# Performance work log

Measured on AMD Instinct MI355X. Metric: run time of the kernel, lower is better.

## Reference

```python
import jax, jax.numpy as jnp
import numpy as np
from jax import lax

V, D_IN, H, B, T = 80, 8, 256, 4096, 80
W_SCALE = 1.0 / np.sqrt(H)  # matches torch nn.LSTM uniform init scale


def setup_inputs() -> dict:
    key = jax.random.key(0)
    ks = jax.random.split(key, 8)
    inp = {
        "x": jax.random.randint(ks[0], (B, T), 0, V),
        "h0": jnp.zeros((2, B, H), jnp.float32),
        "c0": jnp.zeros((2, B, H), jnp.float32),
        "emb": jax.random.normal(ks[1], (V, D_IN), jnp.float32),
        "W_ih0": jax.random.normal(ks[2], (4 * H, D_IN), jnp.float32) * W_SCALE,
        "W_hh0": jax.random.normal(ks[3], (4 * H, H), jnp.float32) * W_SCALE,
        "W_ih1": jax.random.normal(ks[4], (4 * H, H), jnp.float32) * W_SCALE,
        "W_hh1": jax.random.normal(ks[5], (4 * H, H), jnp.float32) * W_SCALE,
        "fc_W": jax.random.normal(ks[6], (V, H), jnp.float32) * W_SCALE,
        "fc_b": jnp.zeros((V,), jnp.float32),
    }
    return inp


def _lstm_layer(xs, h0, c0, W_ih, W_hh):
    # xs: [T, B, d_in]; precompute input contribution for all timesteps at once
    x_gates = jnp.einsum("tbd,gd->tbg", xs, W_ih)  # [T, B, 4H]

    def step(carry, xg):
        h, c = carry
        gates = xg + h @ W_hh.T  # [B, 4H], torch gate order i,f,g,o
        i, f, g, o = jnp.split(gates, 4, axis=-1)
        c = jax.nn.sigmoid(f) * c + jax.nn.sigmoid(i) * jnp.tanh(g)
        h = jax.nn.sigmoid(o) * jnp.tanh(c)
        return (h, c), h

    (hT, cT), hs = lax.scan(step, (h0, c0), x_gates)
    return hs, hT, cT  # hs: [T, B, H]


def reference(x, h0, c0, emb, W_ih0, W_hh0, W_ih1, W_hh1, fc_W, fc_b):
    xe = emb[x]                     # [B, T, D_IN] embedding lookup
    xs = jnp.swapaxes(xe, 0, 1)     # [T, B, D_IN] time-major for scan
    h1s, h1T, c1T = _lstm_layer(xs, h0[0], c0[0], W_ih0, W_hh0)
    h2s, h2T, c2T = _lstm_layer(h1s, h0[1], c0[1], W_ih1, W_hh1)
    logits = h2s[-1] @ fc_W.T + fc_b            # fc on last timestep: [B, V]
    h_n = jnp.stack([h1T, h2T])                  # [2, B, H]
    c_n = jnp.stack([c1T, c2T])
    return logits, h_n, c_n
```

## Files before the change

kernel.cpp:

```cpp
#include <hip/hip_runtime.h>
#include <hip/hip_bf16.h>
#include <stdint.h>

typedef __bf16 bf16x8 __attribute__((ext_vector_type(8)));
typedef float  f32x4  __attribute__((ext_vector_type(4)));

#define MFMA16(a, b, c) __builtin_amdgcn_mfma_f32_16x16x32_bf16((a), (b), (c), 0, 0, 0)

namespace {
constexpr int T_   = 80;
constexpr int B_   = 4096;
constexpr int H_   = 256;
constexpr int HP_  = 264;
constexpr int V_   = 80;
constexpr int RF   = 16;
constexpr int RC   = 32;
constexpr int NH   = 128;
constexpr int NTILE = 128;
constexpr int OUT_HN = B_ * V_;
constexpr int OUT_CN = OUT_HN + 2 * B_ * H_;

constexpr size_t WB_WHH0 = 0;
constexpr size_t WB_WIH1 = (size_t)1 << 20;
constexpr size_t WB_WHH1 = (size_t)2 << 20;
constexpr size_t WB_WIH0 = (size_t)3 << 20;
constexpr int WS_PLANE = 794624;
constexpr size_t WSB_XCHG  = 3178496;
constexpr size_t XCHG_U32  = (size_t)RC * NH;
constexpr size_t WSB_FLAGS = WSB_XCHG + (size_t)2 * 2 * NTILE * 2 * XCHG_U32 * 4;
constexpr int    CTRL_U32  = 512 + 256 + 8;
constexpr size_t WSB_TOTAL = WSB_FLAGS + (size_t)CTRL_U32 * 4;
}

__device__ __forceinline__ float sigm_(float x) { return 1.0f / (1.0f + __expf(-x)); }
__device__ __forceinline__ float tanh_(float x) {
  x = fminf(fmaxf(x, -15.f), 15.f);
  float e = __expf(2.f * x);
  return (e - 1.f) / (e + 1.f);
}

__device__ __forceinline__ void split_(float w, __hip_bfloat16* hi, __hip_bfloat16* lo) {
  __hip_bfloat16 h = __float2bfloat16(w);
  *hi = h;
  *lo = __float2bfloat16(w - __bfloat162float(h));
}

__device__ __forceinline__ uint32_t pack2_(__hip_bfloat16 hi, __hip_bfloat16 lo) {
  return (uint32_t)__builtin_bit_cast(unsigned short, hi) |
         ((uint32_t)__builtin_bit_cast(unsigned short, lo) << 16);
}
__device__ __forceinline__ __hip_bfloat16 ubf_(unsigned short v) {
  return __builtin_bit_cast(__hip_bfloat16, v);
}

__device__ __forceinline__ void ldfrag_(const char* pp, bf16x8* h, bf16x8* l) {
  *h = *(const bf16x8*)pp;
  *l = *(const bf16x8*)(pp + 16);
}

__device__ __forceinline__ size_t addrK256_(int e) {
  int row = e >> 8, kk = e & 255;
  int g = row >> 8, cb = row & 255, t = cb >> 4, m = cb & 15;
  int k = kk >> 5, quad = (kk >> 3) & 3, j = kk & 7;
  return (size_t)(((t * 8 + k) * 4 + g)) * 2048 + (size_t)((quad * 16 + m) * 32 + j * 2);
}

__global__ __launch_bounds__(256) void cvt_pair(
    const float* __restrict__ Wih0f, const float* __restrict__ Whh0f,
    const float* __restrict__ Wih1f, const float* __restrict__ Whh1f,
    __hip_bfloat16* __restrict__ ws, int zero_flags)
{
  if (zero_flags && blockIdx.x < 4) {
    uint32_t* fl = (uint32_t*)((char*)ws + WSB_FLAGS);
    int idx = blockIdx.x * 256 + threadIdx.x;
    if (idx < CTRL_U32) fl[idx] = 0u;
  }
  int i = blockIdx.x * 256 + threadIdx.x;
  if (i >= WS_PLANE) return;
  char* wb = (char*)ws;
  float v; size_t off;
  if (i < 262144) {
    v = Whh0f[i];            off = WB_WHH0 + addrK256_(i);
  } else if (i < 524288) {
    int e = i - 262144;
    v = Wih1f[e];            off = WB_WIH1 + addrK256_(e);
  } else if (i < 786432) {
    int e = i - 524288;
    v = Whh1f[e];            off = WB_WHH1 + addrK256_(e);
  } else {
    int e = i - 786432;
    int row = e >> 3, j = e & 7;
    int g = row >> 8, cb = row & 255, t = cb >> 4, m = cb & 15;
    v = Wih0f[e];
    off = WB_WIH0 + (size_t)((t * 4 + g) * 512 + m * 32 + j * 2);
  }
  __hip_bfloat16 hi = __float2bfloat16(v);
  *(__hip_bfloat16*)(wb + off)      = hi;
  *(__hip_bfloat16*)(wb + off + 16) = __float2bfloat16(v - __bfloat162float(hi));
}

__device__ __forceinline__ f32x4 tri_(bf16x8 ahi, bf16x8 alo, bf16x8 bhi, bf16x8 blo, f32x4 acc) {
  acc = MFMA16(ahi, bhi, acc);
  acc = MFMA16(ahi, blo, acc);
  acc = MFMA16(alo, bhi, acc);
  return acc;
}

__global__ __attribute__((amdgpu_waves_per_eu(2, 2))) __launch_bounds__(512)
void lstm_coop(
    const int* __restrict__ x,
    const float* __restrict__ h0,
    const float* __restrict__ c0,
    const float* __restrict__ emb,
    const __hip_bfloat16* __restrict__ wsW,
    const float* __restrict__ fcW,
    const float* __restrict__ fcb,
    float* __restrict__ out)
{
  __shared__ __align__(16) __hip_bfloat16 h1s[2][2][RC][HP_];
  __shared__ __align__(16) __hip_bfloat16 h2s[2][RC][HP_];
  __shared__ __align__(16) __hip_bfloat16 embs[2][V_][8];
  __shared__ unsigned short toks[RC][T_];
  __shared__ int slot_s;

  const int tid  = threadIdx.x;
  const int lane = tid & 63;
  const int wv   = tid >> 6;
  const int m    = lane & 15;
  const int quad = lane >> 4;
  const int jw   = wv * 16;
  const int lane32 = lane << 5;

  uint32_t* xch   = (uint32_t*)((char*)wsW + WSB_XCHG);
  uint32_t* flags = (uint32_t*)((char*)wsW + WSB_FLAGS);
  uint32_t* owner = flags + 512;
  uint32_t* cnt   = flags + 768;

  if (tid == 0) {
    uint32_t xcd;
    asm volatile("s_getreg_b32 %0, hwreg(20, 0, 4)" : "=s"(xcd));
    xcd &= 7u;
    uint32_t rank = atomicAdd(&cnt[xcd], 1u) & 31u;
    int p = (int)((xcd * 32u + rank) & 255u);
    while (atomicCAS(&owner[p], 0u, 1u) != 0u) p = (p + 1) & 255;
    slot_s = p;
  }
  __syncthreads();
  const int slot = slot_s;
  const int vx   = slot >> 5;
  const int rank = slot & 31;
  const int half = vx >> 2;
  const int tile = (vx & 3) * 32 + rank;
  const int r0   = tile * RC;
  const int oh   = half ^ 1;
  const int colb = half * NH + jw + m;
  const int tcol = half * 8 + wv;

  const char* wb    = (const char*)wsW;
  const char* pWhh0 = wb + WB_WHH0;
  const char* pWih1 = wb + WB_WIH1;
  const char* pWhh1 = wb + WB_WHH1;
  const char* pWih0 = wb + WB_WIH0;

  uint32_t* fl_own  = flags + half * NTILE + tile;
  uint32_t* fl_prt  = flags + oh   * NTILE + tile;
  uint32_t* fl_own1 = flags + 2 * NTILE + half * NTILE + tile;
  uint32_t* fl_prt1 = flags + 2 * NTILE + oh   * NTILE + tile;

  uint32_t* xo0 = xch + (((size_t)(0 * 2 + half) * NTILE + tile) * 2) * XCHG_U32;
  const uint32_t* xi0 = xch + (((size_t)(0 * 2 + oh) * NTILE + tile) * 2) * XCHG_U32;
  uint32_t* xo1 = xch + (((size_t)(1 * 2 + half) * NTILE + tile) * 2) * XCHG_U32;
  const uint32_t* xi1 = xch + (((size_t)(1 * 2 + oh) * NTILE + tile) * 2) * XCHG_U32;

  if (tid < V_) {
#pragma unroll
    for (int j = 0; j < 8; ++j)
      split_(emb[tid * 8 + j], &embs[0][tid][j], &embs[1][tid][j]);
  }
  for (int i = tid; i < RC * T_; i += 512) {
    int r = i / T_, tt = i - r * T_;
    int tok = x[(r0 + r) * T_ + tt];
    toks[r][tt] = (unsigned short)(tok < 0 ? 0 : (tok >= V_ ? V_ - 1 : tok));
  }
  for (int i = tid; i < RC * H_; i += 512) {
    int r = i >> 8, cc = i & 255;
    split_(h0[(0 * B_ + r0 + r) * H_ + cc], &h1s[1][0][r][cc], &h1s[1][1][r][cc]);
    split_(h0[(1 * B_ + r0 + r) * H_ + cc], &h2s[0][r][cc],    &h2s[1][r][cc]);
  }
  f32x4 c1[2], c2[2];
#pragma unroll
  for (int mt = 0; mt < 2; ++mt)
#pragma unroll
    for (int r = 0; r < 4; ++r) {
      int row = r0 + mt * 16 + quad * 4 + r;
      c1[mt][r] = c0[(0 * B_ + row) * H_ + colb];
      c2[mt][r] = c0[(1 * B_ + row) * H_ + colb];
    }

  bf16x8 zb;
#pragma unroll
  for (int j = 0; j < 8; ++j) zb[j] = (__bf16)0.0f;
  const f32x4 zf = {0.f, 0.f, 0.f, 0.f};

  __syncthreads();

  for (int t = 0; t < T_; ++t) {
    const int p = t & 1, q = p ^ 1;

    f32x4 acc[2][4];
    bf16x8 B0h[2][4], B0l[2][4];
#pragma unroll
    for (int g = 0; g < 4; ++g)
      ldfrag_(pWhh0 + ((size_t)((tcol * 8 + 0) * 4 + g) << 11) + lane32,
              &B0h[0][g], &B0l[0][g]);
    {
      bf16x8 eh0 = zb, el0 = zb, eh1 = zb, el1 = zb;
      if (quad == 0) {
        int t0 = toks[m][t], t1 = toks[16 + m][t];
        eh0 = *(const bf16x8*)&embs[0][t0][0]; el0 = *(const bf16x8*)&embs[1][t0][0];
        eh1 = *(const bf16x8*)&embs[0][t1][0]; el1 = *(const bf16x8*)&embs[1][t1][0];
      }
#pragma unroll
      for (int g = 0; g < 4; ++g) {
        bf16x8 Bh, Bl;
        ldfrag_(pWih0 + (size_t)((tcol * 4 + g) * 512 + (m << 5)), &Bh, &Bl);
        acc[0][g] = tri_(eh0, el0, Bh, Bl, zf);
        acc[1][g] = tri_(eh1, el1, Bh, Bl, zf);
      }
    }
#pragma unroll
    for (int k = 0; k < 8; ++k) {
      const int kb = k & 1, kn = kb ^ 1;
      if (k < 7) {
#pragma unroll
        for (int g = 0; g < 4; ++g)
          ldfrag_(pWhh0 + ((size_t)((tcol * 8 + k + 1) * 4 + g) << 11) + lane32,
                  &B0h[kn][g], &B0l[kn][g]);
      }
      const int ko = k * 32 + quad * 8;
      bf16x8 Ah0 = *(const bf16x8*)&h1s[q][0][m][ko];
      bf16x8 Al0 = *(const bf16x8*)&h1s[q][1][m][ko];
      bf16x8 Ah1 = *(const bf16x8*)&h1s[q][0][16 + m][ko];
      bf16x8 Al1 = *(const bf16x8*)&h1s[q][1][16 + m][ko];
#pragma unroll
      for (int g = 0; g < 4; ++g) {
        acc[0][g] = tri_(Ah0, Al0, B0h[kb][g], B0l[kb][g], acc[0][g]);
        acc[1][g] = tri_(Ah1, Al1, B0h[kb][g], B0l[kb][g], acc[1][g]);
      }
    }

    bf16x8 W1h[2][4], W1l[2][4];
#pragma unroll
    for (int g = 0; g < 4; ++g)
      ldfrag_(pWhh1 + ((size_t)((tcol * 8 + 0) * 4 + g) << 11) + lane32,
              &W1h[0][g], &W1l[0][g]);

    {
      uint32_t* xo = xo0 + (size_t)p * XCHG_U32;
#pragma unroll
      for (int mt = 0; mt < 2; ++mt)
#pragma unroll
        for (int r = 0; r < 4; ++r) {
          float ig = sigm_(acc[mt][0][r]);
          float fg = sigm_(acc[mt][1][r]);
          float gg = tanh_(acc[mt][2][r]);
          float og = sigm_(acc[mt][3][r]);
          float cn = fg * c1[mt][r] + ig * gg;
          c1[mt][r] = cn;
          float hv = og * tanh_(cn);
          int rr = mt * 16 + quad * 4 + r;
          __hip_bfloat16 hi, lo;
          split_(hv, &hi, &lo);
          h1s[p][0][rr][colb] = hi;
          h1s[p][1][rr][colb] = lo;
          __hip_atomic_store(&xo[rr * NH + jw + m], pack2_(hi, lo),
                             __ATOMIC_RELAXED, __HIP_MEMORY_SCOPE_AGENT);
        }
    }
    __syncthreads();
    if (tid == 0) {
      __hip_atomic_store(fl_own, (uint32_t)(t + 1),
                         __ATOMIC_RELAXED, __HIP_MEMORY_SCOPE_AGENT);
      while (__hip_atomic_load(fl_prt1, __ATOMIC_RELAXED,
                               __HIP_MEMORY_SCOPE_AGENT) < (uint32_t)t)
        __builtin_amdgcn_s_sleep(2);
    }
    __syncthreads();
    if (t > 0) {
      const uint64_t* xj = (const uint64_t*)(xi1 + (size_t)q * XCHG_U32);
      for (int i = tid; i < RC * NH / 2; i += 512) {
        uint64_t u = __hip_atomic_load(&xj[i], __ATOMIC_RELAXED, __HIP_MEMORY_SCOPE_AGENT);
        int row = i >> 6, c2 = (i & 63) * 2;
        uint32_t w0 = (uint32_t)u, w1 = (uint32_t)(u >> 32);
        h2s[0][row][oh * NH + c2]     = ubf_((unsigned short)(w0 & 0xffffu));
        h2s[1][row][oh * NH + c2]     = ubf_((unsigned short)(w0 >> 16));
        h2s[0][row][oh * NH + c2 + 1] = ubf_((unsigned short)(w1 & 0xffffu));
        h2s[1][row][oh * NH + c2 + 1] = ubf_((unsigned short)(w1 >> 16));
      }
    }
    __syncthreads();

#pragma unroll
    for (int mt = 0; mt < 2; ++mt)
#pragma unroll
      for (int g = 0; g < 4; ++g) acc[mt][g] = zf;
#pragma unroll
    for (int k = 0; k < 8; ++k) {
      const int kb = k & 1, kn = kb ^ 1;
      if (k < 7) {
#pragma unroll
        for (int g = 0; g < 4; ++g)
          ldfrag_(pWhh1 + ((size_t)((tcol * 8 + k + 1) * 4 + g) << 11) + lane32,
                  &W1h[kn][g], &W1l[kn][g]);
      }
      const int ko = k * 32 + quad * 8;
      bf16x8 Ch0 = *(const bf16x8*)&h2s[0][m][ko];
      bf16x8 Cl0 = *(const bf16x8*)&h2s[1][m][ko];
      bf16x8 Ch1 = *(const bf16x8*)&h2s[0][16 + m][ko];
      bf16x8 Cl1 = *(const bf16x8*)&h2s[1][16 + m][ko];
#pragma unroll
      for (int g = 0; g < 4; ++g) {
        acc[0][g] = tri_(Ch0, Cl0, W1h[kb][g], W1l[kb][g], acc[0][g]);
        acc[1][g] = tri_(Ch1, Cl1, W1h[kb][g], W1l[kb][g], acc[1][g]);
      }
    }

    bf16x8 W2h[2][4], W2l[2][4];
#pragma unroll
    for (int g = 0; g < 4; ++g)
      ldfrag_(pWih1 + ((size_t)((tcol * 8 + 0) * 4 + g) << 11) + lane32,
              &W2h[0][g], &W2l[0][g]);

    if (tid == 0) {
      while (__hip_atomic_load(fl_prt, __ATOMIC_RELAXED,
                               __HIP_MEMORY_SCOPE_AGENT) < (uint32_t)(t + 1))
        __builtin_amdgcn_s_sleep(2);
    }
    __syncthreads();
    {
      const uint64_t* xi = (const uint64_t*)(xi0 + (size_t)p * XCHG_U32);
      for (int i = tid; i < RC * NH / 2; i += 512) {
        uint64_t u = __hip_atomic_load(&xi[i], __ATOMIC_RELAXED, __HIP_MEMORY_SCOPE_AGENT);
        int row = i >> 6, c2 = (i & 63) * 2;
        uint32_t w0 = (uint32_t)u, w1 = (uint32_t)(u >> 32);
        h1s[p][0][row][oh * NH + c2]     = ubf_((unsigned short)(w0 & 0xffffu));
        h1s[p][1][row][oh * NH + c2]     = ubf_((unsigned short)(w0 >> 16));
        h1s[p][0][row][oh * NH + c2 + 1] = ubf_((unsigned short)(w1 & 0xffffu));
        h1s[p][1][row][oh * NH + c2 + 1] = ubf_((unsigned short)(w1 >> 16));
      }
    }
    __syncthreads();

#pragma unroll
    for (int k = 0; k < 8; ++k) {
      const int kb = k & 1, kn = kb ^ 1;
      if (k < 7) {
#pragma unroll
        for (int g = 0; g < 4; ++g)
          ldfrag_(pWih1 + ((size_t)((tcol * 8 + k + 1) * 4 + g) << 11) + lane32,
                  &W2h[kn][g], &W2l[kn][g]);
      }
      const int ko = k * 32 + quad * 8;
      bf16x8 Ah0 = *(const bf16x8*)&h1s[p][0][m][ko];
      bf16x8 Al0 = *(const bf16x8*)&h1s[p][1][m][ko];
      bf16x8 Ah1 = *(const bf16x8*)&h1s[p][0][16 + m][ko];
      bf16x8 Al1 = *(const bf16x8*)&h1s[p][1][16 + m][ko];
#pragma unroll
      for (int g = 0; g < 4; ++g) {
        acc[0][g] = tri_(Ah0, Al0, W2h[kb][g], W2l[kb][g], acc[0][g]);
        acc[1][g] = tri_(Ah1, Al1, W2h[kb][g], W2l[kb][g], acc[1][g]);
      }
    }

    {
      uint32_t* xo = xo1 + (size_t)p * XCHG_U32;
#pragma unroll
      for (int mt = 0; mt < 2; ++mt)
#pragma unroll
        for (int r = 0; r < 4; ++r) {
          float ig = sigm_(acc[mt][0][r]);
          float fg = sigm_(acc[mt][1][r]);
          float gg = tanh_(acc[mt][2][r]);
          float og = sigm_(acc[mt][3][r]);
          float cn = fg * c2[mt][r] + ig * gg;
          c2[mt][r] = cn;
          float hv = og * tanh_(cn);
          int rr = mt * 16 + quad * 4 + r;
          __hip_bfloat16 hi, lo;
          split_(hv, &hi, &lo);
          h2s[0][rr][colb] = hi;
          h2s[1][rr][colb] = lo;
          __hip_atomic_store(&xo[rr * NH + jw + m], pack2_(hi, lo),
                             __ATOMIC_RELAXED, __HIP_MEMORY_SCOPE_AGENT);
        }
    }
    __syncthreads();
    if (tid == 0)
      __hip_atomic_store(fl_own1, (uint32_t)(t + 1),
                         __ATOMIC_RELAXED, __HIP_MEMORY_SCOPE_AGENT);
  }

  if (tid == 0) {
    while (__hip_atomic_load(fl_prt1, __ATOMIC_RELAXED,
                             __HIP_MEMORY_SCOPE_AGENT) < (uint32_t)T_)
      __builtin_amdgcn_s_sleep(2);
  }
  __syncthreads();
  {
    const uint64_t* xj = (const uint64_t*)(xi1 + (size_t)((T_ - 1) & 1) * XCHG_U32);
    for (int i = tid; i < RC * NH / 2; i += 512) {
      uint64_t u = __hip_atomic_load(&xj[i], __ATOMIC_RELAXED, __HIP_MEMORY_SCOPE_AGENT);
      int row = i >> 6, c2 = (i & 63) * 2;
      uint32_t w0 = (uint32_t)u, w1 = (uint32_t)(u >> 32);
      h2s[0][row][oh * NH + c2]     = ubf_((unsigned short)(w0 & 0xffffu));
      h2s[1][row][oh * NH + c2]     = ubf_((unsigned short)(w0 >> 16));
      h2s[0][row][oh * NH + c2 + 1] = ubf_((unsigned short)(w1 & 0xffffu));
      h2s[1][row][oh * NH + c2 + 1] = ubf_((unsigned short)(w1 >> 16));
    }
  }
  __syncthreads();

  const int pf = (T_ - 1) & 1;

  for (int i = tid; i < RC * NH; i += 512) {
    int r = i >> 7, c = i & (NH - 1), col = half * NH + c;
    out[OUT_HN + (0 * B_ + r0 + r) * H_ + col] =
        __bfloat162float(h1s[pf][0][r][col]) + __bfloat162float(h1s[pf][1][r][col]);
    out[OUT_HN + (1 * B_ + r0 + r) * H_ + col] =
        __bfloat162float(h2s[0][r][col]) + __bfloat162float(h2s[1][r][col]);
  }
#pragma unroll
  for (int mt = 0; mt < 2; ++mt)
#pragma unroll
    for (int r = 0; r < 4; ++r) {
      int row = r0 + mt * 16 + quad * 4 + r;
      out[OUT_CN + row * H_ + colb]           = c1[mt][r];
      out[OUT_CN + B_ * H_ + row * H_ + colb] = c2[mt][r];
    }
  for (int i = tid; i < RC * (V_ / 2); i += 512) {
    int r = i / (V_ / 2), v = half * (V_ / 2) + i % (V_ / 2);
    const float* wp = fcW + v * H_;
    float s = fcb[v];
#pragma unroll 8
    for (int k = 0; k < H_; ++k) {
      float hk = __bfloat162float(h2s[0][r][k]) + __bfloat162float(h2s[1][r][k]);
      s += hk * wp[k];
    }
    out[(r0 + r) * V_ + v] = s;
  }
}

template<bool USE_WS>
__device__ __forceinline__ void loadB_(const char* wtb, int grp, int lane,
                                       const float* wf, int off,
                                       bf16x8* bhi, bf16x8* blo) {
  if (USE_WS) {
    const char* pp = wtb + ((size_t)grp << 11) + (lane << 5);
    *bhi = *(const bf16x8*)pp;
    *blo = *(const bf16x8*)(pp + 16);
  } else {
    f32x4 a = *(const f32x4*)(wf + off);
    f32x4 b = *(const f32x4*)(wf + off + 4);
#pragma unroll
    for (int j = 0; j < 4; ++j) {
      float w = a[j]; __bf16 h = (__bf16)w;
      (*bhi)[j] = h; (*blo)[j] = (__bf16)(w - (float)h);
    }
#pragma unroll
    for (int j = 0; j < 4; ++j) {
      float w = b[j]; __bf16 h = (__bf16)w;
      (*bhi)[4 + j] = h; (*blo)[4 + j] = (__bf16)(w - (float)h);
    }
  }
}

template<bool USE_WS>
__global__ __launch_bounds__(512, 2) void lstm_fused(
    const int* __restrict__ x,
    const float* __restrict__ h0,
    const float* __restrict__ c0,
    const float* __restrict__ emb,
    const __hip_bfloat16* __restrict__ wsW,
    const float* __restrict__ Wih0f,
    const float* __restrict__ Whh0f,
    const float* __restrict__ Wih1f,
    const float* __restrict__ Whh1f,
    const float* __restrict__ fcW,
    const float* __restrict__ fcb,
    float* __restrict__ out)
{
  __shared__ __align__(16) __hip_bfloat16 h1s[2][2][RF][HP_];
  __shared__ __align__(16) __hip_bfloat16 h2s[2][RF][HP_];
  __shared__ __align__(16) __hip_bfloat16 embs[2][V_][8];
  __shared__ __align__(16) __hip_bfloat16 es[2][RF][8];

  const int tid  = threadIdx.x;
  const int lane = tid & 63;
  const int wv   = tid >> 6;
  const int m    = lane & 15;
  const int quad = lane >> 4;
  const int jw   = wv * 32;
  const int r0   = blockIdx.x * RF;
  const char* wb = (const char*)wsW;

  if (tid < V_) {
#pragma unroll
    for (int j = 0; j < 8; ++j)
      split_(emb[tid * 8 + j], &embs[0][tid][j], &embs[1][tid][j]);
  }
  for (int i = tid; i < RF * H_; i += 512) {
    int r = i >> 8, cc = i & 255;
    split_(h0[(0 * B_ + r0 + r) * H_ + cc], &h1s[1][0][r][cc], &h1s[1][1][r][cc]);
    split_(h0[(1 * B_ + r0 + r) * H_ + cc], &h2s[0][r][cc],    &h2s[1][r][cc]);
  }
  f32x4 c1[2], c2[2];
#pragma unroll
  for (int ct = 0; ct < 2; ++ct)
#pragma unroll
    for (int r = 0; r < 4; ++r) {
      int row = r0 + quad * 4 + r;
      int col = jw + ct * 16 + m;
      c1[ct][r] = c0[(0 * B_ + row) * H_ + col];
      c2[ct][r] = c0[(1 * B_ + row) * H_ + col];
    }

  bf16x8 zb;
#pragma unroll
  for (int j = 0; j < 8; ++j) zb[j] = (__bf16)0.0f;
  const f32x4 zf = {0.f, 0.f, 0.f, 0.f};

  __syncthreads();

  for (int t = 0; t < T_; ++t) {
    const int p = t & 1, q = p ^ 1;

    if (tid < RF) {
      int tok = x[(r0 + tid) * T_ + t];
      tok = tok < 0 ? 0 : (tok >= V_ ? V_ - 1 : tok);
      *(bf16x8*)&es[0][tid][0] = *(const bf16x8*)&embs[0][tok][0];
      *(bf16x8*)&es[1][tid][0] = *(const bf16x8*)&embs[1][tok][0];
    }
    __syncthreads();

    f32x4 acc[8];
    {
      bf16x8 eh = zb, el = zb;
      if (quad == 0) {
        eh = *(const bf16x8*)&es[0][m][0];
        el = *(const bf16x8*)&es[1][m][0];
      }
#pragma unroll
      for (int g = 0; g < 4; ++g)
#pragma unroll
        for (int ct = 0; ct < 2; ++ct) {
          bf16x8 Bh = zb, Bl = zb;
          if (quad == 0) {
            if (USE_WS) {
              const char* pp = wb + WB_WIH0 +
                               (size_t)(((wv * 2 + ct) * 4 + g) * 512 + (m << 5));
              Bh = *(const bf16x8*)pp;
              Bl = *(const bf16x8*)(pp + 16);
            } else {
              const int off = (g * 256 + jw + ct * 16 + m) * 8;
              loadB_<false>(nullptr, 0, 0, Wih0f, off, &Bh, &Bl);
            }
          }
          acc[g * 2 + ct] = tri_(eh, el, Bh, Bl, zf);
        }
    }
#pragma unroll
    for (int k = 0; k < 8; ++k) {
      const int ko = k * 32 + quad * 8;
      bf16x8 Ah = *(const bf16x8*)&h1s[q][0][m][ko];
      bf16x8 Al = *(const bf16x8*)&h1s[q][1][m][ko];
#pragma unroll
      for (int g = 0; g < 4; ++g)
#pragma unroll
        for (int ct = 0; ct < 2; ++ct) {
          bf16x8 Bh, Bl;
          const int grp = ((wv * 2 + ct) * 8 + k) * 4 + g;
          const int off = (g * 256 + jw + ct * 16 + m) * H_ + ko;
          loadB_<USE_WS>(wb + WB_WHH0, grp, lane, Whh0f, off, &Bh, &Bl);
          acc[g * 2 + ct] = tri_(Ah, Al, Bh, Bl, acc[g * 2 + ct]);
        }
    }
#pragma unroll
    for (int ct = 0; ct < 2; ++ct)
#pragma unroll
      for (int r = 0; r < 4; ++r) {
        float ig = sigm_(acc[0 + ct][r]);
        float fg = sigm_(acc[2 + ct][r]);
        float gg = tanh_(acc[4 + ct][r]);
        float og = sigm_(acc[6 + ct][r]);
        float cn = fg * c1[ct][r] + ig * gg;
        c1[ct][r] = cn;
        float hv = og * tanh_(cn);
        int rr = quad * 4 + r, col = jw + ct * 16 + m;
        split_(hv, &h1s[p][0][rr][col], &h1s[p][1][rr][col]);
      }
    __syncthreads();

#pragma unroll
    for (int nt = 0; nt < 8; ++nt) acc[nt] = zf;
#pragma unroll
    for (int k = 0; k < 8; ++k) {
      const int ko = k * 32 + quad * 8;
      bf16x8 Ah = *(const bf16x8*)&h1s[p][0][m][ko];
      bf16x8 Al = *(const bf16x8*)&h1s[p][1][m][ko];
      bf16x8 Ch = *(const bf16x8*)&h2s[0][m][ko];
      bf16x8 Cl = *(const bf16x8*)&h2s[1][m][ko];
#pragma unroll
      for (int g = 0; g < 4; ++g)
#pragma unroll
        for (int ct = 0; ct < 2; ++ct) {
          const int grp = ((wv * 2 + ct) * 8 + k) * 4 + g;
          const int off = (g * 256 + jw + ct * 16 + m) * H_ + ko;
          bf16x8 Bh, Bl;
          loadB_<USE_WS>(wb + WB_WIH1, grp, lane, Wih1f, off, &Bh, &Bl);
          acc[g * 2 + ct] = tri_(Ah, Al, Bh, Bl, acc[g * 2 + ct]);
          loadB_<USE_WS>(wb + WB_WHH1, grp, lane, Whh1f, off, &Bh, &Bl);
          acc[g * 2 + ct] = tri_(Ch, Cl, Bh, Bl, acc[g * 2 + ct]);
        }
    }
    __syncthreads();

#pragma unroll
    for (int ct = 0; ct < 2; ++ct)
#pragma unroll
      for (int r = 0; r < 4; ++r) {
        float ig = sigm_(acc[0 + ct][r]);
        float fg = sigm_(acc[2 + ct][r]);
        float gg = tanh_(acc[4 + ct][r]);
        float og = sigm_(acc[6 + ct][r]);
        float cn = fg * c2[ct][r] + ig * gg;
        c2[ct][r] = cn;
        float hv = og * tanh_(cn);
        int rr = quad * 4 + r, col = jw + ct * 16 + m;
        split_(hv, &h2s[0][rr][col], &h2s[1][rr][col]);
      }
  }
  __syncthreads();

  const int pf = (T_ - 1) & 1;

  for (int i = tid; i < RF * H_; i += 512) {
    int r = i >> 8, cc = i & 255;
    out[OUT_HN + (0 * B_ + r0 + r) * H_ + cc] =
        __bfloat162float(h1s[pf][0][r][cc]) + __bfloat162float(h1s[pf][1][r][cc]);
    out[OUT_HN + (1 * B_ + r0 + r) * H_ + cc] =
        __bfloat162float(h2s[0][r][cc]) + __bfloat162float(h2s[1][r][cc]);
  }
#pragma unroll
  for (int ct = 0; ct < 2; ++ct)
#pragma unroll
    for (int r = 0; r < 4; ++r) {
      int row = r0 + quad * 4 + r;
      int col = jw + ct * 16 + m;
      out[OUT_CN + row * H_ + col]           = c1[ct][r];
      out[OUT_CN + B_ * H_ + row * H_ + col] = c2[ct][r];
    }
  for (int i = tid; i < RF * V_; i += 512) {
    int r = i / V_, v = i - r * V_;
    const float* wp = fcW + v * H_;
    float s = fcb[v];
#pragma unroll 8
    for (int k = 0; k < H_; ++k) {
      float hk = __bfloat162float(h2s[0][r][k]) + __bfloat162float(h2s[1][r][k]);
      s += hk * wp[k];
    }
    out[(r0 + r) * V_ + v] = s;
  }
}

extern "C" void kernel_launch(void* const* d_in, const int* in_sizes, int n_in,
                              void* d_out, int out_size, void* d_ws, size_t ws_size,
                              hipStream_t stream) {
  (void)in_sizes; (void)n_in; (void)out_size;
  const int*   x    = (const int*)d_in[0];
  const float* h0   = (const float*)d_in[1];
  const float* c0   = (const float*)d_in[2];
  const float* emb  = (const float*)d_in[3];
  const float* Wih0 = (const float*)d_in[4];
  const float* Whh0 = (const float*)d_in[5];
  const float* Wih1 = (const float*)d_in[6];
  const float* Whh1 = (const float*)d_in[7];
  const float* fcW  = (const float*)d_in[8];
  const float* fcb  = (const float*)d_in[9];
  float* outp = (float*)d_out;

  __hip_bfloat16* wsW = (__hip_bfloat16*)d_ws;

  if (ws_size >= WSB_TOTAL) {
    cvt_pair<<<(WS_PLANE + 255) / 256, 256, 0, stream>>>(Wih0, Whh0, Wih1, Whh1, wsW, 1);
    void* args[] = { (void*)&x, (void*)&h0, (void*)&c0, (void*)&emb, (void*)&wsW,
                     (void*)&fcW, (void*)&fcb, (void*)&outp };
    hipLaunchCooperativeKernel(reinterpret_cast<void*>(lstm_coop),
                               dim3(256), dim3(512), args, 0, stream);
  } else if (ws_size >= WSB_XCHG) {
    cvt_pair<<<(WS_PLANE + 255) / 256, 256, 0, stream>>>(Wih0, Whh0, Wih1, Whh1, wsW, 0);
    lstm_fused<true><<<B_ / RF, 512, 0, stream>>>(
        x, h0, c0, emb, wsW, Wih0, Whh0, Wih1, Whh1, fcW, fcb, outp);
  } else {
    lstm_fused<false><<<B_ / RF, 512, 0, stream>>>(
        x, h0, c0, emb, wsW, Wih0, Whh0, Wih1, Whh1, fcW, fcb, outp);
  }
}
```

Baseline: 3.064 ms.

## Split hidden dimension across four cooperating blocks with 64-row batch tiles

The work split changes from pairs of blocks that each own half of the hidden columns for 32 batch rows to groups of four blocks that each own a quarter of the columns for 64 rows. Each wave now covers 16 columns and 32 rows, so every block reuses each weight fragment across twice as many rows. Each block now waits on and reads state from three peers instead of one, which adds cross-block flag traffic and exchange reads. The h1 shared buffer is no longer double-buffered, so an extra barrier is added before it is overwritten.

```diff
diff --git a/kernel.cpp b/kernel.cpp
--- a/kernel.cpp
+++ b/kernel.cpp
@@ -14,9 +14,9 @@
 constexpr int HP_  = 264;
 constexpr int V_   = 80;
 constexpr int RF   = 16;
-constexpr int RC   = 32;
-constexpr int NH   = 128;
-constexpr int NTILE = 128;
+constexpr int RC   = 64;
+constexpr int NQ   = 64;
+constexpr int NT   = 64;
 constexpr int OUT_HN = B_ * V_;
 constexpr int OUT_CN = OUT_HN + 2 * B_ * H_;
 
@@ -26,8 +26,7 @@
 constexpr size_t WB_WIH0 = (size_t)3 << 20;
 constexpr int WS_PLANE = 794624;
 constexpr size_t WSB_XCHG  = 3178496;
-constexpr size_t XCHG_U32  = (size_t)RC * NH;
-constexpr size_t WSB_FLAGS = WSB_XCHG + (size_t)2 * 2 * NTILE * 2 * XCHG_U32 * 4;
+constexpr size_t WSB_FLAGS = WSB_XCHG + (size_t)2 * 4 * NT * 2 * 4096 * 4;
 constexpr int    CTRL_U32  = 512 + 256 + 8;
 constexpr size_t WSB_TOTAL = WSB_FLAGS + (size_t)CTRL_U32 * 4;
 }
@@ -106,6 +105,36 @@
   return acc;
 }
 
+__device__ __forceinline__ void spin3_(uint32_t* flags, int tn, int quarter, int tile,
+                                       uint32_t target, int tid) {
+  if (tid < 3) {
+    int qq = tid < quarter ? tid : tid + 1;
+    while (__hip_atomic_load(&flags[tn * 256 + qq * NT + tile],
+                             __ATOMIC_RELAXED, __HIP_MEMORY_SCOPE_AGENT) < target)
+      __builtin_amdgcn_s_sleep(2);
+  }
+}
+
+__device__ __forceinline__ void xread3_(const uint32_t* xch, int tn, int quarter,
+                                        int tile, int par, int tid,
+                                        __hip_bfloat16 (*d0)[HP_],
+                                        __hip_bfloat16 (*d1)[HP_]) {
+  for (int i = tid; i < 3 * 2048; i += 512) {
+    int pi = i >> 11;
+    int qq = pi < quarter ? pi : pi + 1;
+    int j  = i & 2047;
+    const uint64_t* xj = (const uint64_t*)(xch +
+        (((size_t)(tn * 4 + qq) * NT + tile) * 2 + par) * 4096);
+    uint64_t u = __hip_atomic_load(&xj[j], __ATOMIC_RELAXED, __HIP_MEMORY_SCOPE_AGENT);
+    int row = j >> 5, cc = qq * NQ + ((j & 31) << 1);
+    uint32_t w0 = (uint32_t)u, w1 = (uint32_t)(u >> 32);
+    d0[row][cc]     = ubf_((unsigned short)(w0 & 0xffffu));
+    d1[row][cc]     = ubf_((unsigned short)(w0 >> 16));
+    d0[row][cc + 1] = ubf_((unsigned short)(w1 & 0xffffu));
+    d1[row][cc + 1] = ubf_((unsigned short)(w1 >> 16));
+  }
+}
+
 __global__ __attribute__((amdgpu_waves_per_eu(2, 2))) __launch_bounds__(512)
 void lstm_coop(
     const int* __restrict__ x,
@@ -117,7 +146,7 @@
     const float* __restrict__ fcb,
     float* __restrict__ out)
 {
-  __shared__ __align__(16) __hip_bfloat16 h1s[2][2][RC][HP_];
+  __shared__ __align__(16) __hip_bfloat16 h1s[2][RC][HP_];
   __shared__ __align__(16) __hip_bfloat16 h2s[2][RC][HP_];
   __shared__ __align__(16) __hip_bfloat16 embs[2][V_][8];
   __shared__ unsigned short toks[RC][T_];
@@ -128,7 +157,9 @@
   const int wv   = tid >> 6;
   const int m    = lane & 15;
   const int quad = lane >> 4;
-  const int jw   = wv * 16;
+  const int ct   = wv & 3;
+  const int rh   = wv >> 2;
+  const int rbase = rh * 32;
   const int lane32 = lane << 5;
 
   uint32_t* xch   = (uint32_t*)((char*)wsW + WSB_XCHG);
@@ -149,12 +180,11 @@
   const int slot = slot_s;
   const int vx   = slot >> 5;
   const int rank = slot & 31;
-  const int half = vx >> 2;
-  const int tile = (vx & 3) * 32 + rank;
+  const int quarter = vx >> 1;
+  const int tile = (vx & 1) * 32 + rank;
   const int r0   = tile * RC;
-  const int oh   = half ^ 1;
-  const int colb = half * NH + jw + m;
-  const int tcol = half * 8 + wv;
+  const int colb = quarter * NQ + ct * 16 + m;
+  const int tcol = quarter * 4 + ct;
 
   const char* wb    = (const char*)wsW;
   const char* pWhh0 = wb + WB_WHH0;
@@ -162,15 +192,11 @@
   const char* pWhh1 = wb + WB_WHH1;
   const char* pWih0 = wb + WB_WIH0;
 
-  uint32_t* fl_own  = flags + half * NTILE + tile;
-  uint32_t* fl_prt  = flags + oh   * NTILE + tile;
-  uint32_t* fl_own1 = flags + 2 * NTILE + half * NTILE + tile;
-  uint32_t* fl_prt1 = flags + 2 * NTILE + oh   * NTILE + tile;
-
-  uint32_t* xo0 = xch + (((size_t)(0 * 2 + half) * NTILE + tile) * 2) * XCHG_U32;
-  const uint32_t* xi0 = xch + (((size_t)(0 * 2 + oh) * NTILE + tile) * 2) * XCHG_U32;
-  uint32_t* xo1 = xch + (((size_t)(1 * 2 + half) * NTILE + tile) * 2) * XCHG_U32;
-  const uint32_t* xi1 = xch + (((size_t)(1 * 2 + oh) * NTILE + tile) * 2) * XCHG_U32;
+  uint32_t* fl_h1_own = flags + 0 * 256 + quarter * NT + tile;
+  uint32_t* fl_h2_own = flags + 1 * 256 + quarter * NT + tile;
+
+  uint32_t* xo0 = xch + (((size_t)(0 * 4 + quarter) * NT + tile) * 2) * 4096;
+  uint32_t* xo1 = xch + (((size_t)(1 * 4 + quarter) * NT + tile) * 2) * 4096;
 
   if (tid < V_) {
 #pragma unroll
@@ -184,15 +210,15 @@
   }
   for (int i = tid; i < RC * H_; i += 512) {
     int r = i >> 8, cc = i & 255;
-    split_(h0[(0 * B_ + r0 + r) * H_ + cc], &h1s[1][0][r][cc], &h1s[1][1][r][cc]);
-    split_(h0[(1 * B_ + r0 + r) * H_ + cc], &h2s[0][r][cc],    &h2s[1][r][cc]);
+    split_(h0[(0 * B_ + r0 + r) * H_ + cc], &h1s[0][r][cc], &h1s[1][r][cc]);
+    split_(h0[(1 * B_ + r0 + r) * H_ + cc], &h2s[0][r][cc], &h2s[1][r][cc]);
   }
   f32x4 c1[2], c2[2];
 #pragma unroll
   for (int mt = 0; mt < 2; ++mt)
 #pragma unroll
     for (int r = 0; r < 4; ++r) {
-      int row = r0 + mt * 16 + quad * 4 + r;
+      int row = r0 + rbase + mt * 16 + quad * 4 + r;
       c1[mt][r] = c0[(0 * B_ + row) * H_ + colb];
       c2[mt][r] = c0[(1 * B_ + row) * H_ + colb];
     }
@@ -216,7 +242,7 @@
     {
       bf16x8 eh0 = zb, el0 = zb, eh1 = zb, el1 = zb;
       if (quad == 0) {
-        int t0 = toks[m][t], t1 = toks[16 + m][t];
+        int t0 = toks[rbase + m][t], t1 = toks[rbase + 16 + m][t];
         eh0 = *(const bf16x8*)&embs[0][t0][0]; el0 = *(const bf16x8*)&embs[1][t0][0];
         eh1 = *(const bf16x8*)&embs[0][t1][0]; el1 = *(const bf16x8*)&embs[1][t1][0];
       }
@@ -238,10 +264,10 @@
                   &B0h[kn][g], &B0l[kn][g]);
       }
       const int ko = k * 32 + quad * 8;
-      bf16x8 Ah0 = *(const bf16x8*)&h1s[q][0][m][ko];
-      bf16x8 Al0 = *(const bf16x8*)&h1s[q][1][m][ko];
-      bf16x8 Ah1 = *(const bf16x8*)&h1s[q][0][16 + m][ko];
-      bf16x8 Al1 = *(const bf16x8*)&h1s[q][1][16 + m][ko];
+      bf16x8 Ah0 = *(const bf16x8*)&h1s[0][rbase + m][ko];
+      bf16x8 Al0 = *(const bf16x8*)&h1s[1][rbase + m][ko];
+      bf16x8 Ah1 = *(const bf16x8*)&h1s[0][rbase + 16 + m][ko];
+      bf16x8 Al1 = *(const bf16x8*)&h1s[1][rbase + 16 + m][ko];
 #pragma unroll
       for (int g = 0; g < 4; ++g) {
         acc[0][g] = tri_(Ah0, Al0, B0h[kb][g], B0l[kb][g], acc[0][g]);
@@ -255,8 +281,10 @@
       ldfrag_(pWhh1 + ((size_t)((tcol * 8 + 0) * 4 + g) << 11) + lane32,
               &W1h[0][g], &W1l[0][g]);
 
+    __syncthreads();
+
     {
-      uint32_t* xo = xo0 + (size_t)p * XCHG_U32;
+      uint32_t* xo = xo0 + (size_t)p * 4096;
 #pragma unroll
       for (int mt = 0; mt < 2; ++mt)
 #pragma unroll
@@ -268,36 +296,23 @@
           float cn = fg * c1[mt][r] + ig * gg;
           c1[mt][r] = cn;
           float hv = og * tanh_(cn);
-          int rr = mt * 16 + quad * 4 + r;
+          int rr = rbase + mt * 16 + quad * 4 + r;
           __hip_bfloat16 hi, lo;
           split_(hv, &hi, &lo);
-          h1s[p][0][rr][colb] = hi;
-          h1s[p][1][rr][colb] = lo;
-          __hip_atomic_store(&xo[rr * NH + jw + m], pack2_(hi, lo),
+          h1s[0][rr][colb] = hi;
+          h1s[1][rr][colb] = lo;
+          __hip_atomic_store(&xo[rr * NQ + ct * 16 + m], pack2_(hi, lo),
                              __ATOMIC_RELAXED, __HIP_MEMORY_SCOPE_AGENT);
         }
     }
     __syncthreads();
-    if (tid == 0) {
-      __hip_atomic_store(fl_own, (uint32_t)(t + 1),
+    if (tid == 0)
+      __hip_atomic_store(fl_h1_own, (uint32_t)(t + 1),
                          __ATOMIC_RELAXED, __HIP_MEMORY_SCOPE_AGENT);
-      while (__hip_atomic_load(fl_prt1, __ATOMIC_RELAXED,
-                               __HIP_MEMORY_SCOPE_AGENT) < (uint32_t)t)
-        __builtin_amdgcn_s_sleep(2);
-    }
-    __syncthreads();
-    if (t > 0) {
-      const uint64_t* xj = (const uint64_t*)(xi1 + (size_t)q * XCHG_U32);
-      for (int i = tid; i < RC * NH / 2; i += 512) {
-        uint64_t u = __hip_atomic_load(&xj[i], __ATOMIC_RELAXED, __HIP_MEMORY_SCOPE_AGENT);
-        int row = i >> 6, c2 = (i & 63) * 2;
-        uint32_t w0 = (uint32_t)u, w1 = (uint32_t)(u >> 32);
-        h2s[0][row][oh * NH + c2]     = ubf_((unsigned short)(w0 & 0xffffu));
-        h2s[1][row][oh * NH + c2]     = ubf_((unsigned short)(w0 >> 16));
-        h2s[0][row][oh * NH + c2 + 1] = ubf_((unsigned short)(w1 & 0xffffu));
-        h2s[1][row][oh * NH + c2 + 1] = ubf_((unsigned short)(w1 >> 16));
-      }
-    }
+    spin3_(flags, 1, quarter, tile, (uint32_t)t, tid);
+    __syncthreads();
+    if (t > 0)
+      xread3_(xch, 1, quarter, tile, q, tid, h2s[0], h2s[1]);
     __syncthreads();
 
 #pragma unroll
@@ -314,10 +329,10 @@
                   &W1h[kn][g], &W1l[kn][g]);
       }
       const int ko = k * 32 + quad * 8;
-      bf16x8 Ch0 = *(const bf16x8*)&h2s[0][m][ko];
-      bf16x8 Cl0 = *(const bf16x8*)&h2s[1][m][ko];
-      bf16x8 Ch1 = *(const bf16x8*)&h2s[0][16 + m][ko];
-      bf16x8 Cl1 = *(const bf16x8*)&h2s[1][16 + m][ko];
+      bf16x8 Ch0 = *(const bf16x8*)&h2s[0][rbase + m][ko];
+      bf16x8 Cl0 = *(const bf16x8*)&h2s[1][rbase + m][ko];
+      bf16x8 Ch1 = *(const bf16x8*)&h2s[0][rbase + 16 + m][ko];
+      bf16x8 Cl1 = *(const bf16x8*)&h2s[1][rbase + 16 + m][ko];
 #pragma unroll
       for (int g = 0; g < 4; ++g) {
         acc[0][g] = tri_(Ch0, Cl0, W1h[kb][g], W1l[kb][g], acc[0][g]);
@@ -331,24 +346,9 @@
       ldfrag_(pWih1 + ((size_t)((tcol * 8 + 0) * 4 + g) << 11) + lane32,
               &W2h[0][g], &W2l[0][g]);
 
-    if (tid == 0) {
-      while (__hip_atomic_load(fl_prt, __ATOMIC_RELAXED,
-                               __HIP_MEMORY_SCOPE_AGENT) < (uint32_t)(t + 1))
-        __builtin_amdgcn_s_sleep(2);
-    }
-    __syncthreads();
-    {
-      const uint64_t* xi = (const uint64_t*)(xi0 + (size_t)p * XCHG_U32);
-      for (int i = tid; i < RC * NH / 2; i += 512) {
-        uint64_t u = __hip_atomic_load(&xi[i], __ATOMIC_RELAXED, __HIP_MEMORY_SCOPE_AGENT);
-        int row = i >> 6, c2 = (i & 63) * 2;
-        uint32_t w0 = (uint32_t)u, w1 = (uint32_t)(u >> 32);
-        h1s[p][0][row][oh * NH + c2]     = ubf_((unsigned short)(w0 & 0xffffu));
-        h1s[p][1][row][oh * NH + c2]     = ubf_((unsigned short)(w0 >> 16));
-        h1s[p][0][row][oh * NH + c2 + 1] = ubf_((unsigned short)(w1 & 0xffffu));
-        h1s[p][1][row][oh * NH + c2 + 1] = ubf_((unsigned short)(w1 >> 16));
-      }
-    }
+    spin3_(flags, 0, quarter, tile, (uint32_t)(t + 1), tid);
+    __syncthreads();
+    xread3_(xch, 0, quarter, tile, p, tid, h1s[0], h1s[1]);
     __syncthreads();
 
 #pragma unroll
@@ -361,10 +361,10 @@
                   &W2h[kn][g], &W2l[kn][g]);
       }
       const int ko = k * 32 + quad * 8;
-      bf16x8 Ah0 = *(const bf16x8*)&h1s[p][0][m][ko];
-      bf16x8 Al0 = *(const bf16x8*)&h1s[p][1][m][ko];
-      bf16x8 Ah1 = *(const bf16x8*)&h1s[p][0][16 + m][ko];
-      bf16x8 Al1 = *(const bf16x8*)&h1s[p][1][16 + m][ko];
+      bf16x8 Ah0 = *(const bf16x8*)&h1s[0][rbase + m][ko];
+      bf16x8 Al0 = *(const bf16x8*)&h1s[1][rbase + m][ko];
+      bf16x8 Ah1 = *(const bf16x8*)&h1s[0][rbase + 16 + m][ko];
+      bf16x8 Al1 = *(const bf16x8*)&h1s[1][rbase + 16 + m][ko];
 #pragma unroll
       for (int g = 0; g < 4; ++g) {
         acc[0][g] = tri_(Ah0, Al0, W2h[kb][g], W2l[kb][g], acc[0][g]);
@@ -373,7 +373,7 @@
     }
 
     {
-      uint32_t* xo = xo1 + (size_t)p * XCHG_U32;
+      uint32_t* xo = xo1 + (size_t)p * 4096;
 #pragma unroll
       for (int mt = 0; mt < 2; ++mt)
 #pragma unroll
@@ -385,47 +385,30 @@
           float cn = fg * c2[mt][r] + ig * gg;
           c2[mt][r] = cn;
           float hv = og * tanh_(cn);
-          int rr = mt * 16 + quad * 4 + r;
+          int rr = rbase + mt * 16 + quad * 4 + r;
           __hip_bfloat16 hi, lo;
           split_(hv, &hi, &lo);
           h2s[0][rr][colb] = hi;
           h2s[1][rr][colb] = lo;
-          __hip_atomic_store(&xo[rr * NH + jw + m], pack2_(hi, lo),
+          __hip_atomic_store(&xo[rr * NQ + ct * 16 + m], pack2_(hi, lo),
                              __ATOMIC_RELAXED, __HIP_MEMORY_SCOPE_AGENT);
         }
     }
     __syncthreads();
     if (tid == 0)
-      __hip_atomic_store(fl_own1, (uint32_t)(t + 1),
+      __hip_atomic_store(fl_h2_own, (uint32_t)(t + 1),
                          __ATOMIC_RELAXED, __HIP_MEMORY_SCOPE_AGENT);
   }
 
-  if (tid == 0) {
-    while (__hip_atomic_load(fl_prt1, __ATOMIC_RELAXED,
-                             __HIP_MEMORY_SCOPE_AGENT) < (uint32_t)T_)
-      __builtin_amdgcn_s_sleep(2);
-  }
+  spin3_(flags, 1, quarter, tile, (uint32_t)T_, tid);
   __syncthreads();
-  {
-    const uint64_t* xj = (const uint64_t*)(xi1 + (size_t)((T_ - 1) & 1) * XCHG_U32);
-    for (int i = tid; i < RC * NH / 2; i += 512) {
-      uint64_t u = __hip_atomic_load(&xj[i], __ATOMIC_RELAXED, __HIP_MEMORY_SCOPE_AGENT);
-      int row = i >> 6, c2 = (i & 63) * 2;
-      uint32_t w0 = (uint32_t)u, w1 = (uint32_t)(u >> 32);
-      h2s[0][row][oh * NH + c2]     = ubf_((unsigned short)(w0 & 0xffffu));
-      h2s[1][row][oh * NH + c2]     = ubf_((unsigned short)(w0 >> 16));
-      h2s[0][row][oh * NH + c2 + 1] = ubf_((unsigned short)(w1 & 0xffffu));
-      h2s[1][row][oh * NH + c2 + 1] = ubf_((unsigned short)(w1 >> 16));
-    }
-  }
+  xread3_(xch, 1, quarter, tile, (T_ - 1) & 1, tid, h2s[0], h2s[1]);
   __syncthreads();
 
-  const int pf = (T_ - 1) & 1;
-
-  for (int i = tid; i < RC * NH; i += 512) {
-    int r = i >> 7, c = i & (NH - 1), col = half * NH + c;
+  for (int i = tid; i < RC * NQ; i += 512) {
+    int r = i >> 6, c = i & (NQ - 1), col = quarter * NQ + c;
     out[OUT_HN + (0 * B_ + r0 + r) * H_ + col] =
-        __bfloat162float(h1s[pf][0][r][col]) + __bfloat162float(h1s[pf][1][r][col]);
+        __bfloat162float(h1s[0][r][col]) + __bfloat162float(h1s[1][r][col]);
     out[OUT_HN + (1 * B_ + r0 + r) * H_ + col] =
         __bfloat162float(h2s[0][r][col]) + __bfloat162float(h2s[1][r][col]);
   }
@@ -433,12 +416,12 @@
   for (int mt = 0; mt < 2; ++mt)
 #pragma unroll
     for (int r = 0; r < 4; ++r) {
-      int row = r0 + mt * 16 + quad * 4 + r;
+      int row = r0 + rbase + mt * 16 + quad * 4 + r;
       out[OUT_CN + row * H_ + colb]           = c1[mt][r];
       out[OUT_CN + B_ * H_ + row * H_ + colb] = c2[mt][r];
     }
-  for (int i = tid; i < RC * (V_ / 2); i += 512) {
-    int r = i / (V_ / 2), v = half * (V_ / 2) + i % (V_ / 2);
+  for (int i = tid; i < RC * (V_ / 4); i += 512) {
+    int r = i / (V_ / 4), v = quarter * (V_ / 4) + i % (V_ / 4);
     const float* wp = fcW + v * H_;
     float s = fcb[v];
 #pragma unroll 8
```

Result: slower. 3.417 ms (+11.5%).

## Prefetch partner layer-2 hidden state early and let all threads spin on flags

Applied to the files above, without the earlier changes.

Moves the wait on the partner block's layer-2 flag and the global loads of its hidden-state half to the start of each timestep, holding them in registers. They are written to shared memory only after the layer-1 matmul, which takes one wait/load/barrier phase off the critical path. Every thread now polls the flags itself instead of thread 0 polling followed by a barrier, which removes barriers but adds global flag traffic. Register pressure rises because of the four held 64-bit values.

```diff
diff --git a/kernel.cpp b/kernel.cpp
--- a/kernel.cpp
+++ b/kernel.cpp
@@ -207,6 +207,18 @@
   for (int t = 0; t < T_; ++t) {
     const int p = t & 1, q = p ^ 1;
 
+    uint64_t hreg[4];
+    if (t > 0) {
+      while (__hip_atomic_load(fl_prt1, __ATOMIC_RELAXED,
+                               __HIP_MEMORY_SCOPE_AGENT) < (uint32_t)t)
+        __builtin_amdgcn_s_sleep(2);
+      const uint64_t* xj = (const uint64_t*)(xi1 + (size_t)q * XCHG_U32);
+#pragma unroll
+      for (int j = 0; j < 4; ++j)
+        hreg[j] = __hip_atomic_load(&xj[tid + j * 512], __ATOMIC_RELAXED,
+                                    __HIP_MEMORY_SCOPE_AGENT);
+    }
+
     f32x4 acc[2][4];
     bf16x8 B0h[2][4], B0l[2][4];
 #pragma unroll
@@ -254,6 +266,18 @@
     for (int g = 0; g < 4; ++g)
       ldfrag_(pWhh1 + ((size_t)((tcol * 8 + 0) * 4 + g) << 11) + lane32,
               &W1h[0][g], &W1l[0][g]);
+
+    if (t > 0) {
+#pragma unroll
+      for (int j = 0; j < 4; ++j) {
+        int i = tid + j * 512, row = i >> 6, cc = (i & 63) * 2;
+        uint32_t w0 = (uint32_t)hreg[j], w1 = (uint32_t)(hreg[j] >> 32);
+        h2s[0][row][oh * NH + cc]     = ubf_((unsigned short)(w0 & 0xffffu));
+        h2s[1][row][oh * NH + cc]     = ubf_((unsigned short)(w0 >> 16));
+        h2s[0][row][oh * NH + cc + 1] = ubf_((unsigned short)(w1 & 0xffffu));
+        h2s[1][row][oh * NH + cc + 1] = ubf_((unsigned short)(w1 >> 16));
+      }
+    }
 
     {
       uint32_t* xo = xo0 + (size_t)p * XCHG_U32;
@@ -278,27 +302,9 @@
         }
     }
     __syncthreads();
-    if (tid == 0) {
+    if (tid == 0)
       __hip_atomic_store(fl_own, (uint32_t)(t + 1),
                          __ATOMIC_RELAXED, __HIP_MEMORY_SCOPE_AGENT);
-      while (__hip_atomic_load(fl_prt1, __ATOMIC_RELAXED,
-                               __HIP_MEMORY_SCOPE_AGENT) < (uint32_t)t)
-        __builtin_amdgcn_s_sleep(2);
-    }
-    __syncthreads();
-    if (t > 0) {
-      const uint64_t* xj = (const uint64_t*)(xi1 + (size_t)q * XCHG_U32);
-      for (int i = tid; i < RC * NH / 2; i += 512) {
-        uint64_t u = __hip_atomic_load(&xj[i], __ATOMIC_RELAXED, __HIP_MEMORY_SCOPE_AGENT);
-        int row = i >> 6, c2 = (i & 63) * 2;
-        uint32_t w0 = (uint32_t)u, w1 = (uint32_t)(u >> 32);
-        h2s[0][row][oh * NH + c2]     = ubf_((unsigned short)(w0 & 0xffffu));
-        h2s[1][row][oh * NH + c2]     = ubf_((unsigned short)(w0 >> 16));
-        h2s[0][row][oh * NH + c2 + 1] = ubf_((unsigned short)(w1 & 0xffffu));
-        h2s[1][row][oh * NH + c2 + 1] = ubf_((unsigned short)(w1 >> 16));
-      }
-    }
-    __syncthreads();
 
 #pragma unroll
     for (int mt = 0; mt < 2; ++mt)
@@ -331,22 +337,21 @@
       ldfrag_(pWih1 + ((size_t)((tcol * 8 + 0) * 4 + g) << 11) + lane32,
               &W2h[0][g], &W2l[0][g]);
 
-    if (tid == 0) {
+    {
       while (__hip_atomic_load(fl_prt, __ATOMIC_RELAXED,
                                __HIP_MEMORY_SCOPE_AGENT) < (uint32_t)(t + 1))
         __builtin_amdgcn_s_sleep(2);
-    }
-    __syncthreads();
-    {
       const uint64_t* xi = (const uint64_t*)(xi0 + (size_t)p * XCHG_U32);
-      for (int i = tid; i < RC * NH / 2; i += 512) {
-        uint64_t u = __hip_atomic_load(&xi[i], __ATOMIC_RELAXED, __HIP_MEMORY_SCOPE_AGENT);
-        int row = i >> 6, c2 = (i & 63) * 2;
+#pragma unroll
+      for (int j = 0; j < 4; ++j) {
+        uint64_t u = __hip_atomic_load(&xi[tid + j * 512], __ATOMIC_RELAXED,
+                                       __HIP_MEMORY_SCOPE_AGENT);
+        int i = tid + j * 512, row = i >> 6, cc = (i & 63) * 2;
         uint32_t w0 = (uint32_t)u, w1 = (uint32_t)(u >> 32);
-        h1s[p][0][row][oh * NH + c2]     = ubf_((unsigned short)(w0 & 0xffffu));
-        h1s[p][1][row][oh * NH + c2]     = ubf_((unsigned short)(w0 >> 16));
-        h1s[p][0][row][oh * NH + c2 + 1] = ubf_((unsigned short)(w1 & 0xffffu));
-        h1s[p][1][row][oh * NH + c2 + 1] = ubf_((unsigned short)(w1 >> 16));
+        h1s[p][0][row][oh * NH + cc]     = ubf_((unsigned short)(w0 & 0xffffu));
+        h1s[p][1][row][oh * NH + cc]     = ubf_((unsigned short)(w0 >> 16));
+        h1s[p][0][row][oh * NH + cc + 1] = ubf_((unsigned short)(w1 & 0xffffu));
+        h1s[p][1][row][oh * NH + cc + 1] = ubf_((unsigned short)(w1 >> 16));
       }
     }
     __syncthreads();
@@ -400,22 +405,21 @@
                          __ATOMIC_RELAXED, __HIP_MEMORY_SCOPE_AGENT);
   }
 
-  if (tid == 0) {
+  {
     while (__hip_atomic_load(fl_prt1, __ATOMIC_RELAXED,
                              __HIP_MEMORY_SCOPE_AGENT) < (uint32_t)T_)
       __builtin_amdgcn_s_sleep(2);
-  }
-  __syncthreads();
-  {
     const uint64_t* xj = (const uint64_t*)(xi1 + (size_t)((T_ - 1) & 1) * XCHG_U32);
-    for (int i = tid; i < RC * NH / 2; i += 512) {
-      uint64_t u = __hip_atomic_load(&xj[i], __ATOMIC_RELAXED, __HIP_MEMORY_SCOPE_AGENT);
-      int row = i >> 6, c2 = (i & 63) * 2;
+#pragma unroll
+    for (int j = 0; j < 4; ++j) {
+      uint64_t u = __hip_atomic_load(&xj[tid + j * 512], __ATOMIC_RELAXED,
+                                     __HIP_MEMORY_SCOPE_AGENT);
+      int i = tid + j * 512, row = i >> 6, cc = (i & 63) * 2;
       uint32_t w0 = (uint32_t)u, w1 = (uint32_t)(u >> 32);
-      h2s[0][row][oh * NH + c2]     = ubf_((unsigned short)(w0 & 0xffffu));
-      h2s[1][row][oh * NH + c2]     = ubf_((unsigned short)(w0 >> 16));
-      h2s[0][row][oh * NH + c2 + 1] = ubf_((unsigned short)(w1 & 0xffffu));
-      h2s[1][row][oh * NH + c2 + 1] = ubf_((unsigned short)(w1 >> 16));
+      h2s[0][row][oh * NH + cc]     = ubf_((unsigned short)(w0 & 0xffffu));
+      h2s[1][row][oh * NH + cc]     = ubf_((unsigned short)(w0 >> 16));
+      h2s[0][row][oh * NH + cc + 1] = ubf_((unsigned short)(w1 & 0xffffu));
+      h2s[1][row][oh * NH + cc + 1] = ubf_((unsigned short)(w1 >> 16));
     }
   }
   __syncthreads();
```

Measured after the change: 3.366 ms. +9.8%, slower.
